# Performance work log

Measured on AMD Instinct MI355X. Metric: run time of the kernel, lower is better.

The kernel has to match this reference:

```python
import jax, jax.numpy as jnp
import numpy as np

NUM_HEADS = 4
EPS = 1e-5


def conv1(W, b, z):
    # Conv1d with kernel_size=1 == channel-wise linear: (B, Cin, L) -> (B, Cout, L)
    return jnp.einsum('oi,bil->bol', W, z) + b[None, :, None]


def setup_inputs() -> dict:
    key = jax.random.key(0)
    ks = jax.random.split(key, 16)
    B, D, N = 2, 256, 4096
    s = 0.05
    return {
        'x': jax.random.normal(ks[0], (B, D, N), jnp.float32),
        'source': jax.random.normal(ks[1], (B, D, N), jnp.float32),
        'Wq': jax.random.normal(ks[2], (D, D), jnp.float32) * s,
        'bq': jax.random.normal(ks[3], (D,), jnp.float32) * s,
        'Wk': jax.random.normal(ks[4], (D, D), jnp.float32) * s,
        'bk': jax.random.normal(ks[5], (D,), jnp.float32) * s,
        'Wv': jax.random.normal(ks[6], (D, D), jnp.float32) * s,
        'bv': jax.random.normal(ks[7], (D,), jnp.float32) * s,
        'Wm': jax.random.normal(ks[8], (D, D), jnp.float32) * s,
        'bm': jax.random.normal(ks[9], (D,), jnp.float32) * s,
        'W1': jax.random.normal(ks[10], (2 * D, 2 * D), jnp.float32) * s,
        'b1': jax.random.normal(ks[11], (2 * D,), jnp.float32) * s,
        'W2': jax.random.normal(ks[12], (D, 2 * D), jnp.float32) * s,
        'b2': jax.random.normal(ks[13], (D,), jnp.float32) * s,
    }


def reference(x, source, Wq, bq, Wk, bk, Wv, bv, Wm, bm, W1, b1, W2, b2):
    B, D, N = x.shape
    M = source.shape[2]
    H = NUM_HEADS
    dim = D // H  # per-head dim; torch reshape splits channels as (dim, heads)

    q = conv1(Wq, bq, x).reshape(B, dim, H, N)
    k = conv1(Wk, bk, source).reshape(B, dim, H, M)
    v = conv1(Wv, bv, source).reshape(B, dim, H, M)

    scores = jnp.einsum('bdhn,bdhm->bhnm', q, k) / (dim ** 0.5)
    prob = jax.nn.softmax(scores, axis=-1)
    attn = jnp.einsum('bhnm,bdhm->bdhn', prob, v).reshape(B, D, N)

    message = conv1(Wm, bm, attn)

    h = conv1(W1, b1, jnp.concatenate([x, message], axis=1))
    # InstanceNorm1d (affine=False, biased var over L)
    mu = jnp.mean(h, axis=2, keepdims=True)
    var = jnp.mean((h - mu) ** 2, axis=2, keepdims=True)
    h = jax.nn.relu((h - mu) / jnp.sqrt(var + EPS))
    return conv1(W2, b2, h)
```

## Files before the change

### kernel.cpp

```cpp
#include <hip/hip_runtime.h>
#include <cstdint>
#include <cstddef>


typedef __attribute__((ext_vector_type(8))) short short8;
typedef __attribute__((ext_vector_type(4))) short bf16x4;
typedef __attribute__((ext_vector_type(4))) float floatx4;

union U2 { unsigned int u[2]; bf16x4 s; };

__device__ __forceinline__ unsigned short f2bf(float x) {
  union { float f; unsigned int u; } c; c.f = x;
  unsigned int r = c.u + 0x7FFFu + ((c.u >> 16) & 1u);
  return (unsigned short)(r >> 16);
}
__device__ __forceinline__ float bf2f(unsigned short u) {
  union { unsigned int i; float f; } c; c.i = ((unsigned int)u) << 16; return c.f;
}
__device__ __forceinline__ void gload16(const void* g, void* l) {
  __builtin_amdgcn_global_load_lds(
      (const __attribute__((address_space(1))) unsigned int*)g,
      (__attribute__((address_space(3))) unsigned int*)l, 16, 0, 0);
}
__device__ __forceinline__ unsigned int cvtpk(float lo, float hi) {
  unsigned int r;
  asm("v_cvt_pk_bf16_f32 %0, %1, %2" : "=v"(r) : "v"(lo), "v"(hi));
  return r;
}
__device__ __forceinline__ floatx4 mfma16(bf16x4 a, bf16x4 b, floatx4 c) {
#if __has_builtin(__builtin_amdgcn_mfma_f32_16x16x16bf16_1k)
  return __builtin_amdgcn_mfma_f32_16x16x16bf16_1k(a, b, c, 0, 0, 0);
#else
  asm("v_mfma_f32_16x16x16_bf16 %0, %1, %2, %0" : "+v"(c) : "v"(a), "v"(b));
  return c;
#endif
}

#define LOG2E_8 0.18033688011112042f

__global__ __launch_bounds__(256) void tx_all(
    const float* __restrict__ x, const float* __restrict__ src,
    unsigned short* __restrict__ xb, unsigned short* __restrict__ sb,
    int C, int N)
{
  __shared__ float tile[32][33];
  const int which = blockIdx.z >> 1, b = blockIdx.z & 1;
  const float* X = which ? src : x;
  unsigned short* Y = which ? sb : xb;
  const int n0 = blockIdx.x * 32, c0 = blockIdx.y * 32;
  const int tc = threadIdx.x & 31, tr = threadIdx.x >> 5;
  #pragma unroll
  for (int i = 0; i < 4; ++i)
    tile[tr + i * 8][tc] = X[((size_t)b * C + c0 + tr + i * 8) * N + n0 + tc];
  __syncthreads();
  #pragma unroll
  for (int i = 0; i < 4; ++i)
    Y[((size_t)b * N + n0 + tr + i * 8) * C + c0 + tc] = f2bf(tile[tc][tr + i * 8]);
}

__global__ __launch_bounds__(256) void wprep(
    const float* __restrict__ Wq, const float* __restrict__ Wk,
    const float* __restrict__ Wv, const float* __restrict__ Wm,
    const float* __restrict__ W1, const float* __restrict__ W2,
    const float* __restrict__ bq, const float* __restrict__ bk,
    const float* __restrict__ bv, const float* __restrict__ bm,
    const float* __restrict__ b1, const float* __restrict__ b2,
    unsigned short* __restrict__ wqkv, unsigned short* __restrict__ wm_,
    unsigned short* __restrict__ w1_, unsigned short* __restrict__ w2_,
    float* __restrict__ biasb)
{
  const int bid = blockIdx.x, t = threadIdx.x;
  if (bid < 768) {
    const int idx = bid * 256 + t;
    const int op = idx >> 8, ip = idx & 255;
    const int grp = op >> 8, oo = op & 255;
    const int o = 4 * (oo & 63) + (oo >> 6);
    const float* W = grp == 0 ? Wq : grp == 1 ? Wk : Wv;
    const float sc = grp == 0 ? LOG2E_8 : 1.f;
    wqkv[idx] = f2bf(W[(size_t)o * 256 + ip] * sc);
  } else if (bid < 1024) {
    const int idx = (bid - 768) * 256 + t;
    const int op = idx >> 8, ip = idx & 255;
    const int i2 = 4 * (ip & 63) + (ip >> 6);
    wm_[idx] = f2bf(Wm[(size_t)op * 256 + i2]);
  } else if (bid < 2048) {
    const int idx = (bid - 1024) * 256 + t;
    w1_[idx] = f2bf(W1[idx]);
  } else if (bid < 2560) {
    const int idx = (bid - 2048) * 256 + t;
    w2_[idx] = f2bf(W2[idx]);
  } else {
    const int z = (bid - 2560) * 256 + t;
    if (z < 256)       biasb[z] = bq[4 * (z & 63) + (z >> 6)] * LOG2E_8;
    else if (z < 512)  { const int y = z - 256; biasb[z] = bk[4 * (y & 63) + (y >> 6)]; }
    else if (z < 768)  { const int y = z - 512; biasb[z] = bv[4 * (y & 63) + (y >> 6)]; }
    else if (z < 1024) biasb[z] = bm[z - 768];
    else if (z < 1536) biasb[z] = b1[z - 1024];
    else if (z < 1792) biasb[z] = b2[z - 1536];
  }
}

__global__ __launch_bounds__(256) void gemm128(
    const unsigned short* __restrict__ Wb, const float* __restrict__ bias,
    const unsigned short* __restrict__ X0, const unsigned short* __restrict__ X1,
    void* __restrict__ O0, void* __restrict__ O1, void* __restrict__ O2,
    int Co, int Ci, int Ci0, int N, int variant)
{
  const int n0 = blockIdx.x * 128;
  const int o0 = blockIdx.y * 128;
  const int b  = blockIdx.z;
  const int t  = threadIdx.x;
  const int w = t >> 6, lane = t & 63, qd = lane >> 4, l = lane & 15;
  const int oh = (w >> 1) * 64, nh = (w & 1) * 64;

  __shared__ unsigned short Wl[128 * 64];
  __shared__ unsigned short Xl[128 * 64];

  floatx4 acc[4][4];
  #pragma unroll
  for (int i = 0; i < 4; ++i)
    #pragma unroll
    for (int j = 0; j < 4; ++j) acc[i][j] = (floatx4){0.f, 0.f, 0.f, 0.f};

  for (int k0 = 0; k0 < Ci; k0 += 64) {
    const unsigned short* Xs; int cb, rl;
    if (variant == 1) { Xs = (o0 < 256) ? X0 : X1; cb = k0; rl = Ci; }
    else if (k0 < Ci0) { Xs = X0; cb = k0; rl = Ci0; }
    else               { Xs = X1; cb = k0 - Ci0; rl = Ci - Ci0; }
    __syncthreads();
    #pragma unroll
    for (int i = 0; i < 4; ++i) {
      const int idx = i * 256 + t;
      const int row = idx >> 3, pg = idx & 7, sg = pg ^ (row & 7);
      gload16(&Wb[(size_t)(o0 + row) * Ci + k0 + sg * 8], &Wl[row * 64 + pg * 8]);
      gload16(&Xs[((size_t)b * N + n0 + row) * rl + cb + sg * 8], &Xl[row * 64 + pg * 8]);
    }
    __syncthreads();

    short8 af[4][2], bf[4][2];
    #pragma unroll
    for (int i = 0; i < 4; ++i) {
      const int ar = oh + 16 * i + l;
      af[i][0] = *(const short8*)&Wl[ar * 64 + ((qd ^ (ar & 7))) * 8];
      af[i][1] = *(const short8*)&Wl[ar * 64 + (((4 + qd) ^ (ar & 7))) * 8];
    }
    #pragma unroll
    for (int j = 0; j < 4; ++j) {
      const int br = nh + 16 * j + l;
      bf[j][0] = *(const short8*)&Xl[br * 64 + ((qd ^ (br & 7))) * 8];
      bf[j][1] = *(const short8*)&Xl[br * 64 + (((4 + qd) ^ (br & 7))) * 8];
    }
    #pragma unroll
    for (int i = 0; i < 4; ++i)
      #pragma unroll
      for (int j = 0; j < 4; ++j) {
        acc[i][j] = __builtin_amdgcn_mfma_f32_16x16x32_bf16(af[i][0], bf[j][0], acc[i][j], 0, 0, 0);
        acc[i][j] = __builtin_amdgcn_mfma_f32_16x16x32_bf16(af[i][1], bf[j][1], acc[i][j], 0, 0, 0);
      }
  }

  const int osec = o0 + oh;
  #pragma unroll
  for (int i = 0; i < 4; ++i) {
    const int o4 = o0 + oh + 16 * i + qd * 4;
    const float4 bi = *(const float4*)&bias[o4];
    #pragma unroll
    for (int j = 0; j < 4; ++j) {
      const int n = n0 + nh + 16 * j + l;
      if (variant == 0) {
        unsigned short* C = (unsigned short*)O0;
        ushort4 pk;
        pk.x = f2bf(acc[i][j][0] + bi.x); pk.y = f2bf(acc[i][j][1] + bi.y);
        pk.z = f2bf(acc[i][j][2] + bi.z); pk.w = f2bf(acc[i][j][3] + bi.w);
        *(ushort4*)&C[((size_t)b * N + n) * Co + o4] = pk;
      } else if (variant == 1) {
        if (osec < 256) {
          unsigned short* C = (unsigned short*)O0;
          ushort4 pk;
          pk.x = f2bf(acc[i][j][0] + bi.x); pk.y = f2bf(acc[i][j][1] + bi.y);
          pk.z = f2bf(acc[i][j][2] + bi.z); pk.w = f2bf(acc[i][j][3] + bi.w);
          *(ushort4*)&C[((size_t)b * N + n) * 256 + o4] = pk;
        } else if (osec < 512) {
          unsigned short* C = (unsigned short*)O1;
          ushort4 pk;
          pk.x = f2bf(acc[i][j][0] + bi.x); pk.y = f2bf(acc[i][j][1] + bi.y);
          pk.z = f2bf(acc[i][j][2] + bi.z); pk.w = f2bf(acc[i][j][3] + bi.w);
          *(ushort4*)&C[((size_t)b * N + n) * 256 + (o4 - 256)] = pk;
        } else {
          unsigned short* C = (unsigned short*)O2;
          #pragma unroll
          for (int rg = 0; rg < 4; ++rg) {
            const int op = o4 - 512 + rg, h = op >> 6, d = op & 63;
            C[(((size_t)b * 4 + h) * 64 + d) * N + n] =
                f2bf(acc[i][j][rg] + ((const float*)&bi)[rg]);
          }
        }
      } else {
        float* C = (float*)O0;
        #pragma unroll
        for (int rg = 0; rg < 4; ++rg)
          C[((size_t)b * Co + o4 + rg) * N + n] = acc[i][j][rg] + ((const float*)&bi)[rg];
      }
    }
  }
}

__global__ __launch_bounds__(256) void attn_mfma(
    const unsigned short* __restrict__ qb, const unsigned short* __restrict__ kb,
    const unsigned short* __restrict__ vh, unsigned short* __restrict__ Opart,
    float* __restrict__ liPart, int N)
{
  const int qt = blockIdx.x;
  const int h  = blockIdx.y;
  const int b  = blockIdx.z >> 2, s = blockIdx.z & 3;
  const int n0 = qt * 128;
  const int t  = threadIdx.x;
  const int w = t >> 6, lane = t & 63, qd = lane >> 4, l = lane & 15;

  __shared__ unsigned short Kl[2][64 * 64];
  __shared__ unsigned short Vl[2][64 * 64];

  const unsigned short* qp0 = &qb[((size_t)b * N + n0 + 16 * w + l) * 256 + h * 64];
  const unsigned short* qp1 = qp0 + (size_t)64 * 256;
  short8 bQ[2][2];
  bQ[0][0] = *(const short8*)&qp0[qd * 8];
  bQ[0][1] = *(const short8*)&qp0[32 + qd * 8];
  bQ[1][0] = *(const short8*)&qp1[qd * 8];
  bQ[1][1] = *(const short8*)&qp1[32 + qd * 8];

  floatx4 accO[2][4];
  #pragma unroll
  for (int qs = 0; qs < 2; ++qs)
    #pragma unroll
    for (int ds = 0; ds < 4; ++ds) accO[qs][ds] = (floatx4){0.f, 0.f, 0.f, 0.f};
  float li[2] = {0.f, 0.f};

  const int j0base = s * 1024;

  auto STAGE = [&](int buf, int j0) {
    #pragma unroll
    for (int i = 0; i < 2; ++i) {
      const int idx = i * 256 + t;
      const int row = idx >> 3, pg = idx & 7, sg = pg ^ (row & 7);
      gload16(&kb[((size_t)b * N + j0 + row) * 256 + h * 64 + sg * 8],
              &Kl[buf][row * 64 + pg * 8]);
      gload16(&vh[(((size_t)b * 4 + h) * 64 + row) * N + j0 + sg * 8],
              &Vl[buf][row * 64 + pg * 8]);
    }
  };

  STAGE(0, j0base);

  #pragma unroll 2
  for (int jt = 0; jt < 16; ++jt) {
    const int cur = jt & 1;
    __syncthreads();
    if (jt < 15) STAGE(cur ^ 1, j0base + (jt + 1) * 64);

    short8 kf[4][2];
    #pragma unroll
    for (int js = 0; js < 4; ++js) {
      const int br = 16 * js + l;
      kf[js][0] = *(const short8*)&Kl[cur][br * 64 + ((qd ^ (br & 7))) * 8];
      kf[js][1] = *(const short8*)&Kl[cur][br * 64 + (((4 + qd) ^ (br & 7))) * 8];
    }
    bf16x4 vf[4][4];
    #pragma unroll
    for (int ds = 0; ds < 4; ++ds) {
      const int vr = 16 * ds + l;
      #pragma unroll
      for (int js = 0; js < 4; ++js) {
        const int pg = js * 2 + (qd >> 1);
        vf[ds][js] = *(const bf16x4*)&Vl[cur][vr * 64 + ((pg ^ (vr & 7))) * 8 + (qd & 1) * 4];
      }
    }

    #pragma unroll
    for (int qs = 0; qs < 2; ++qs) {
      floatx4 S[4];
      __builtin_amdgcn_s_setprio(1);
      #pragma unroll
      for (int js = 0; js < 4; ++js) {
        floatx4 a = (floatx4){0.f, 0.f, 0.f, 0.f};
        a = __builtin_amdgcn_mfma_f32_16x16x32_bf16(kf[js][0], bQ[qs][0], a, 0, 0, 0);
        a = __builtin_amdgcn_mfma_f32_16x16x32_bf16(kf[js][1], bQ[qs][1], a, 0, 0, 0);
        S[js] = a;
      }
      __builtin_amdgcn_s_setprio(0);

      bf16x4 pa[4];
      #pragma unroll
      for (int js = 0; js < 4; ++js) {
        const float p0 = __builtin_exp2f(S[js][0]);
        const float p1 = __builtin_exp2f(S[js][1]);
        const float p2 = __builtin_exp2f(S[js][2]);
        const float p3 = __builtin_exp2f(S[js][3]);
        li[qs] += (p0 + p1) + (p2 + p3);
        U2 pu; pu.u[0] = cvtpk(p0, p1); pu.u[1] = cvtpk(p2, p3);
        pa[js] = pu.s;
      }

      __builtin_amdgcn_s_setprio(1);
      #pragma unroll
      for (int ds = 0; ds < 4; ++ds)
        #pragma unroll
        for (int js = 0; js < 4; ++js)
          accO[qs][ds] = mfma16(pa[js], vf[ds][js], accO[qs][ds]);
      __builtin_amdgcn_s_setprio(0);
    }
  }

  const size_t obase = ((((size_t)b * 4 + h) * 4 + s) * 32 + qt) * 128;
  #pragma unroll
  for (int qs = 0; qs < 2; ++qs) {
    float sum = li[qs];
    sum += __shfl_xor(sum, 16);
    sum += __shfl_xor(sum, 32);
    if (qd == 0) liPart[obase + qs * 64 + 16 * w + l] = sum;
    #pragma unroll
    for (int rg = 0; rg < 4; ++rg) {
      const int q = qs * 64 + 16 * w + qd * 4 + rg;
      #pragma unroll
      for (int ds = 0; ds < 4; ++ds)
        Opart[(obase + q) * 64 + 16 * ds + l] = f2bf(accO[qs][ds][rg]);
    }
  }
}

__global__ __launch_bounds__(256) void attn_combine(
    const unsigned short* __restrict__ Opart, const float* __restrict__ liPart,
    unsigned short* __restrict__ atb, int N)
{
  const int qt = blockIdx.x, h = blockIdx.y, b = blockIdx.z;
  const int t = threadIdx.x;
  const int q = t >> 1, d0 = (t & 1) * 32;

  float li = 0.f;
  size_t idx[4];
  #pragma unroll
  for (int s = 0; s < 4; ++s) {
    idx[s] = ((((size_t)b * 4 + h) * 4 + s) * 32 + qt) * 128 + q;
    li += liPart[idx[s]];
  }
  const float inv = 1.f / li;

  float o[32];
  #pragma unroll
  for (int c = 0; c < 32; ++c) o[c] = 0.f;
  #pragma unroll
  for (int s = 0; s < 4; ++s) {
    #pragma unroll
    for (int c4 = 0; c4 < 4; ++c4) {
      const short8 v = *(const short8*)&Opart[idx[s] * 64 + d0 + c4 * 8];
      #pragma unroll
      for (int j = 0; j < 8; ++j) o[c4 * 8 + j] += bf2f((unsigned short)v[j]);
    }
  }
  unsigned short* dst = &atb[((size_t)b * N + qt * 128 + q) * 256 + h * 64 + d0];
  #pragma unroll
  for (int c4 = 0; c4 < 4; ++c4) {
    ushort4 pk;
    pk.x = f2bf(o[c4 * 8 + 0] * inv); pk.y = f2bf(o[c4 * 8 + 1] * inv);
    pk.z = f2bf(o[c4 * 8 + 2] * inv); pk.w = f2bf(o[c4 * 8 + 3] * inv);
    *(ushort4*)&dst[c4 * 8] = pk;
    pk.x = f2bf(o[c4 * 8 + 4] * inv); pk.y = f2bf(o[c4 * 8 + 5] * inv);
    pk.z = f2bf(o[c4 * 8 + 6] * inv); pk.w = f2bf(o[c4 * 8 + 7] * inv);
    *(ushort4*)&dst[c4 * 8 + 4] = pk;
  }
}

__global__ __launch_bounds__(256) void in_stats(
    const unsigned short* __restrict__ H, float* __restrict__ Ps,
    float* __restrict__ Ps2, int N)
{
  const int cg = blockIdx.x, ns = blockIdx.y, b = blockIdx.z, t = threadIdx.x;
  const int c0 = cg * 64 + (t & 7) * 8;
  float s[8] = {}, s2[8] = {};
  #pragma unroll
  for (int i = 0; i < 8; ++i) {
    const int n = ns * 256 + (t >> 3) + i * 32;
    const short8 hv = *(const short8*)&H[((size_t)b * N + n) * 512 + c0];
    #pragma unroll
    for (int j = 0; j < 8; ++j) {
      const float f = bf2f((unsigned short)hv[j]);
      s[j] += f; s2[j] += f * f;
    }
  }
  __shared__ float rs[32][64], rs2[32][64];
  #pragma unroll
  for (int j = 0; j < 8; ++j) {
    rs[t >> 3][(t & 7) * 8 + j] = s[j];
    rs2[t >> 3][(t & 7) * 8 + j] = s2[j];
  }
  __syncthreads();
  if (t < 64) {
    float a = 0.f, a2 = 0.f;
    #pragma unroll
    for (int r = 0; r < 32; ++r) { a += rs[r][t]; a2 += rs2[r][t]; }
    const size_t o = ((size_t)ns * 2 + b) * 512 + cg * 64 + t;
    Ps[o] = a; Ps2[o] = a2;
  }
}

__global__ __launch_bounds__(256) void in_norm(
    unsigned short* __restrict__ H, const float* __restrict__ Ps,
    const float* __restrict__ Ps2, int N)
{
  const int cg = blockIdx.x, ns = blockIdx.y, b = blockIdx.z, t = threadIdx.x;
  __shared__ float muS[64], ivS[64];
  if (t < 64) {
    const int c = cg * 64 + t;
    float s = 0.f, s2 = 0.f;
    for (int k = 0; k < 16; ++k) {
      s  += Ps [((size_t)k * 2 + b) * 512 + c];
      s2 += Ps2[((size_t)k * 2 + b) * 512 + c];
    }
    const float mu = s / (float)N;
    const float var = fmaxf(s2 / (float)N - mu * mu, 0.f);
    muS[t] = mu;
    ivS[t] = rsqrtf(var + 1e-5f);
  }
  __syncthreads();
  const int c0 = cg * 64 + (t & 7) * 8;
  float mu[8], iv[8];
  #pragma unroll
  for (int j = 0; j < 8; ++j) {
    mu[j] = muS[(t & 7) * 8 + j];
    iv[j] = ivS[(t & 7) * 8 + j];
  }
  #pragma unroll
  for (int i = 0; i < 8; ++i) {
    const int n = ns * 256 + (t >> 3) + i * 32;
    unsigned short* p = &H[((size_t)b * N + n) * 512 + c0];
    short8 hv = *(const short8*)p;
    #pragma unroll
    for (int j = 0; j < 8; ++j) {
      const float f = fmaxf((bf2f((unsigned short)hv[j]) - mu[j]) * iv[j], 0.f);
      hv[j] = (short)f2bf(f);
    }
    *(short8*)p = hv;
  }
}

extern "C" void kernel_launch(void* const* d_in, const int* in_sizes, int n_in,
                              void* d_out, int out_size, void* d_ws, size_t ws_size,
                              hipStream_t stream)
{
  const int B = 2, D = 256, N = 4096;

  const float* x   = (const float*)d_in[0];
  const float* src = (const float*)d_in[1];
  const float* Wq  = (const float*)d_in[2];  const float* bq = (const float*)d_in[3];
  const float* Wk  = (const float*)d_in[4];  const float* bk = (const float*)d_in[5];
  const float* Wv  = (const float*)d_in[6];  const float* bv = (const float*)d_in[7];
  const float* Wm  = (const float*)d_in[8];  const float* bm = (const float*)d_in[9];
  const float* W1  = (const float*)d_in[10]; const float* b1 = (const float*)d_in[11];
  const float* W2  = (const float*)d_in[12]; const float* b2 = (const float*)d_in[13];
  float* out = (float*)d_out;

  char* ws = (char*)d_ws;
  const size_t MB = 1u << 20;
  unsigned short* xb  = (unsigned short*)(ws + 0 * MB);
  unsigned short* sb  = (unsigned short*)(ws + 4 * MB);
  unsigned short* qbf = (unsigned short*)(ws + 8 * MB);
  unsigned short* kbf = (unsigned short*)(ws + 12 * MB);
  unsigned short* vhb = (unsigned short*)(ws + 16 * MB);
  unsigned short* atb = (unsigned short*)(ws + 20 * MB);
  unsigned short* Opart = (unsigned short*)(ws + 24 * MB);
  unsigned short* msb = (unsigned short*)(ws + 24 * MB);
  unsigned short* hb  = (unsigned short*)(ws + 28 * MB);
  float* liPart = (float*)(ws + 41 * MB);
  unsigned short* wqkvb = (unsigned short*)(ws + 42 * MB);
  unsigned short* wmb = wqkvb + 768 * 256;
  unsigned short* w1b = wmb + 256 * 256;
  unsigned short* w2b = w1b + 512 * 512;
  float* biasb = (float*)(ws + 44 * MB);
  float* Ps    = biasb + 2048;
  float* Ps2   = Ps + 16 * 2 * 512;

  const dim3 blk(256);

  tx_all<<<dim3(N / 32, D / 32, 2 * B), blk, 0, stream>>>(x, src, xb, sb, D, N);
  wprep<<<dim3(2567), blk, 0, stream>>>(Wq, Wk, Wv, Wm, W1, W2,
                                        bq, bk, bv, bm, b1, b2,
                                        wqkvb, wmb, w1b, w2b, biasb);

  gemm128<<<dim3(N / 128, 6, B), blk, 0, stream>>>(
      wqkvb, biasb, xb, sb, qbf, kbf, vhb, 768, 256, 256, N, 1);

  attn_mfma<<<dim3(N / 128, 4, B * 4), blk, 0, stream>>>(
      qbf, kbf, vhb, Opart, liPart, N);
  attn_combine<<<dim3(N / 128, 4, B), blk, 0, stream>>>(Opart, liPart, atb, N);

  gemm128<<<dim3(N / 128, 2, B), blk, 0, stream>>>(
      wmb, biasb + 768, atb, atb, msb, nullptr, nullptr, 256, 256, 256, N, 0);

  gemm128<<<dim3(N / 128, 4, B), blk, 0, stream>>>(
      w1b, biasb + 1024, xb, msb, hb, nullptr, nullptr, 512, 512, 256, N, 0);

  in_stats<<<dim3(8, 16, B), blk, 0, stream>>>(hb, Ps, Ps2, N);
  in_norm<<<dim3(8, 16, B), blk, 0, stream>>>(hb, Ps, Ps2, N);

  gemm128<<<dim3(N / 128, 2, B), blk, 0, stream>>>(
      w2b, biasb + 1536, hb, hb, out, nullptr, nullptr, 256, 512, 512, N, 2);
}
```

Baseline: 231.4 us.

## Use 16x16x32 MFMA for PV via permlane swaps and compute row sums on MFMA

The attention inner loop now builds 8-element P fragments by exchanging packed bf16 probabilities across lanes with permlane32/16 swaps. This lets the P·V product use 16x16x32 MFMAs instead of twice as many 16x16x16 ones. The softmax denominator is computed by an extra MFMA against a vector of ones rather than by scalar adds plus cross-lane shuffles. The QK^T MFMAs for both query subtiles are interleaved per key block. The aim is to cut MFMA issue count and VALU work, in exchange for extra permlane instructions and a small amount of extra MFMA work for the row sums.

```diff
diff --git a/kernel.cpp b/kernel.cpp
--- a/kernel.cpp
+++ b/kernel.cpp
@@ -4,10 +4,9 @@
 
 
 typedef __attribute__((ext_vector_type(8))) short short8;
-typedef __attribute__((ext_vector_type(4))) short bf16x4;
 typedef __attribute__((ext_vector_type(4))) float floatx4;
 
-union U2 { unsigned int u[2]; bf16x4 s; };
+union U4 { unsigned int u[4]; short8 s; };
 
 __device__ __forceinline__ unsigned short f2bf(float x) {
   union { float f; unsigned int u; } c; c.f = x;
@@ -26,14 +25,6 @@
   unsigned int r;
   asm("v_cvt_pk_bf16_f32 %0, %1, %2" : "=v"(r) : "v"(lo), "v"(hi));
   return r;
-}
-__device__ __forceinline__ floatx4 mfma16(bf16x4 a, bf16x4 b, floatx4 c) {
-#if __has_builtin(__builtin_amdgcn_mfma_f32_16x16x16bf16_1k)
-  return __builtin_amdgcn_mfma_f32_16x16x16bf16_1k(a, b, c, 0, 0, 0);
-#else
-  asm("v_mfma_f32_16x16x16_bf16 %0, %1, %2, %0" : "+v"(c) : "v"(a), "v"(b));
-  return c;
-#endif
 }
 
 #define LOG2E_8 0.18033688011112042f
@@ -228,12 +219,18 @@
   bQ[1][0] = *(const short8*)&qp1[qd * 8];
   bQ[1][1] = *(const short8*)&qp1[32 + qd * 8];
 
+  short8 ones;
+  #pragma unroll
+  for (int i = 0; i < 8; ++i) ones[i] = (short)0x3F80;
+
   floatx4 accO[2][4];
-  #pragma unroll
-  for (int qs = 0; qs < 2; ++qs)
+  floatx4 accLi[2];
+  #pragma unroll
+  for (int qs = 0; qs < 2; ++qs) {
+    accLi[qs] = (floatx4){0.f, 0.f, 0.f, 0.f};
     #pragma unroll
     for (int ds = 0; ds < 4; ++ds) accO[qs][ds] = (floatx4){0.f, 0.f, 0.f, 0.f};
-  float li[2] = {0.f, 0.f};
+  }
 
   const int j0base = s * 1024;
 
@@ -257,74 +254,84 @@
     __syncthreads();
     if (jt < 15) STAGE(cur ^ 1, j0base + (jt + 1) * 64);
 
-    short8 kf[4][2];
+    floatx4 S[2][4];
+    __builtin_amdgcn_s_setprio(1);
     #pragma unroll
     for (int js = 0; js < 4; ++js) {
       const int br = 16 * js + l;
-      kf[js][0] = *(const short8*)&Kl[cur][br * 64 + ((qd ^ (br & 7))) * 8];
-      kf[js][1] = *(const short8*)&Kl[cur][br * 64 + (((4 + qd) ^ (br & 7))) * 8];
-    }
-    bf16x4 vf[4][4];
-    #pragma unroll
-    for (int ds = 0; ds < 4; ++ds) {
-      const int vr = 16 * ds + l;
+      const short8 k0 = *(const short8*)&Kl[cur][br * 64 + ((qd ^ (br & 7))) * 8];
+      const short8 k1 = *(const short8*)&Kl[cur][br * 64 + (((4 + qd) ^ (br & 7))) * 8];
+      floatx4 a0 = (floatx4){0.f, 0.f, 0.f, 0.f};
+      floatx4 a1 = (floatx4){0.f, 0.f, 0.f, 0.f};
+      a0 = __builtin_amdgcn_mfma_f32_16x16x32_bf16(k0, bQ[0][0], a0, 0, 0, 0);
+      a1 = __builtin_amdgcn_mfma_f32_16x16x32_bf16(k0, bQ[1][0], a1, 0, 0, 0);
+      a0 = __builtin_amdgcn_mfma_f32_16x16x32_bf16(k1, bQ[0][1], a0, 0, 0, 0);
+      a1 = __builtin_amdgcn_mfma_f32_16x16x32_bf16(k1, bQ[1][1], a1, 0, 0, 0);
+      S[0][js] = a0; S[1][js] = a1;
+    }
+    __builtin_amdgcn_s_setprio(0);
+
+    unsigned int T[2][2][4];
+    #pragma unroll
+    for (int qs = 0; qs < 2; ++qs) {
+      unsigned int U[4], W[4];
       #pragma unroll
       for (int js = 0; js < 4; ++js) {
-        const int pg = js * 2 + (qd >> 1);
-        vf[ds][js] = *(const bf16x4*)&Vl[cur][vr * 64 + ((pg ^ (vr & 7))) * 8 + (qd & 1) * 4];
+        const float p0 = __builtin_exp2f(S[qs][js][0]);
+        const float p1 = __builtin_exp2f(S[qs][js][1]);
+        const float p2 = __builtin_exp2f(S[qs][js][2]);
+        const float p3 = __builtin_exp2f(S[qs][js][3]);
+        U[js] = cvtpk(p0, p1);
+        W[js] = cvtpk(p2, p3);
       }
-    }
-
-    #pragma unroll
-    for (int qs = 0; qs < 2; ++qs) {
-      floatx4 S[4];
-      __builtin_amdgcn_s_setprio(1);
-      #pragma unroll
-      for (int js = 0; js < 4; ++js) {
-        floatx4 a = (floatx4){0.f, 0.f, 0.f, 0.f};
-        a = __builtin_amdgcn_mfma_f32_16x16x32_bf16(kf[js][0], bQ[qs][0], a, 0, 0, 0);
-        a = __builtin_amdgcn_mfma_f32_16x16x32_bf16(kf[js][1], bQ[qs][1], a, 0, 0, 0);
-        S[js] = a;
+      #pragma unroll
+      for (int js2 = 0; js2 < 2; ++js2) {
+        unsigned int t0 = U[2 * js2], t2 = U[2 * js2 + 1];
+        asm("v_permlane32_swap_b32 %0, %1" : "+v"(t0), "+v"(t2));
+        asm("v_permlane16_swap_b32 %0, %1" : "+v"(t0), "+v"(t2));
+        unsigned int t1 = W[2 * js2], t3 = W[2 * js2 + 1];
+        asm("v_permlane32_swap_b32 %0, %1" : "+v"(t1), "+v"(t3));
+        asm("v_permlane16_swap_b32 %0, %1" : "+v"(t1), "+v"(t3));
+        T[qs][js2][0] = t0; T[qs][js2][1] = t1;
+        T[qs][js2][2] = t2; T[qs][js2][3] = t3;
       }
-      __builtin_amdgcn_s_setprio(0);
-
-      bf16x4 pa[4];
-      #pragma unroll
-      for (int js = 0; js < 4; ++js) {
-        const float p0 = __builtin_exp2f(S[js][0]);
-        const float p1 = __builtin_exp2f(S[js][1]);
-        const float p2 = __builtin_exp2f(S[js][2]);
-        const float p3 = __builtin_exp2f(S[js][3]);
-        li[qs] += (p0 + p1) + (p2 + p3);
-        U2 pu; pu.u[0] = cvtpk(p0, p1); pu.u[1] = cvtpk(p2, p3);
-        pa[js] = pu.s;
+    }
+
+    __builtin_amdgcn_s_setprio(1);
+    #pragma unroll
+    for (int js2 = 0; js2 < 2; ++js2) {
+      short8 vv[4];
+      #pragma unroll
+      for (int ds = 0; ds < 4; ++ds) {
+        const int vr = 16 * ds + l;
+        vv[ds] = *(const short8*)&Vl[cur][vr * 64 + (((4 * js2 + qd) ^ (vr & 7))) * 8];
       }
-
-      __builtin_amdgcn_s_setprio(1);
-      #pragma unroll
-      for (int ds = 0; ds < 4; ++ds)
+      #pragma unroll
+      for (int qs = 0; qs < 2; ++qs) {
+        U4 pu;
+        pu.u[0] = T[qs][js2][0]; pu.u[1] = T[qs][js2][1];
+        pu.u[2] = T[qs][js2][2]; pu.u[3] = T[qs][js2][3];
+        const short8 pa = pu.s;
         #pragma unroll
-        for (int js = 0; js < 4; ++js)
-          accO[qs][ds] = mfma16(pa[js], vf[ds][js], accO[qs][ds]);
-      __builtin_amdgcn_s_setprio(0);
-    }
+        for (int ds = 0; ds < 4; ++ds)
+          accO[qs][ds] = __builtin_amdgcn_mfma_f32_16x16x32_bf16(pa, vv[ds], accO[qs][ds], 0, 0, 0);
+        accLi[qs] = __builtin_amdgcn_mfma_f32_16x16x32_bf16(pa, ones, accLi[qs], 0, 0, 0);
+      }
+    }
+    __builtin_amdgcn_s_setprio(0);
   }
 
   const size_t obase = ((((size_t)b * 4 + h) * 4 + s) * 32 + qt) * 128;
   #pragma unroll
-  for (int qs = 0; qs < 2; ++qs) {
-    float sum = li[qs];
-    sum += __shfl_xor(sum, 16);
-    sum += __shfl_xor(sum, 32);
-    if (qd == 0) liPart[obase + qs * 64 + 16 * w + l] = sum;
+  for (int qs = 0; qs < 2; ++qs)
     #pragma unroll
     for (int rg = 0; rg < 4; ++rg) {
       const int q = qs * 64 + 16 * w + qd * 4 + rg;
       #pragma unroll
       for (int ds = 0; ds < 4; ++ds)
         Opart[(obase + q) * 64 + 16 * ds + l] = f2bf(accO[qs][ds][rg]);
-    }
-  }
+      if (l == 0) liPart[obase + q] = accLi[qs][rg];
+    }
 }
 
 __global__ __launch_bounds__(256) void attn_combine(
```

Result: faster. 220.2 us (-4.8%).
